# Optimization experiments

Hardware: AMD Instinct MI355X
Metric: run time of the kernel (lower is better)

Reference implementation:

```python
import jax, jax.numpy as jnp
import numpy as np

H, W, C = 256, 320, 28
HEADS, DH = 8, 28
K = 8   # DCT patch kernel (hardcoded in SpecDCT.forward)
WS = 8  # local attention window size
EPS = 1e-12


def _dct_mat(N):
    # torch_dct DCT-II with norm=None: X_k = 2 * sum_n x_n cos(pi*(2n+1)k/(2N))
    n = np.arange(N)
    D = 2.0 * np.cos(np.pi * (2.0 * n[None, :] + 1.0) * n[:, None] / (2.0 * N))
    return D.astype(np.float32)

_DHn = _dct_mat(H)
_DWn = _dct_mat(W)
D_H = jnp.asarray(_DHn)
D_W = jnp.asarray(_DWn)
DI_H = jnp.asarray(np.linalg.inv(_DHn).astype(np.float32))
DI_W = jnp.asarray(np.linalg.inv(_DWn).astype(np.float32))


def _l2norm(t):
    return t / jnp.maximum(jnp.linalg.norm(t, axis=-1, keepdims=True), EPS)


def _gelu(t):
    return jax.nn.gelu(t, approximate=False)


def _forward(x, spec_wq, spec_wk, spec_wv, spec_rescale, spec_proj_w, spec_proj_b,
             hf1_pw_w, hf1_dw_w, hf2_pw_w, coef_emb,
             loc_wq, loc_wkv, loc_pos, loc_proj_w, loc_proj_b, fus_w, fus_b):
    b = x.shape[0]
    hh, ww = H // K, W // K
    n = hh * ww
    mm = K * K
    # ---------- spectral DCT branch ----------
    x_nchw = x.transpose(0, 3, 1, 2)                                  # [b,C,H,W]
    x_dct = jnp.einsum('kh,bchw,lw->bckl', D_H, x_nchw, D_W)          # 2D DCT-II
    # patchify into 8x8 DCT blocks -> [b, n, mm, C]
    xt = x_dct.reshape(b, C, hh, K, ww, K).transpose(0, 2, 4, 3, 5, 1).reshape(b, n, mm, C)
    q = (xt @ spec_wq).reshape(b, n, mm, HEADS, DH).transpose(0, 1, 3, 4, 2)  # [b,n,h,d,mm]
    k = (xt @ spec_wk).reshape(b, n, mm, HEADS, DH).transpose(0, 1, 3, 4, 2)
    v = (xt @ spec_wv).reshape(b, n, mm, HEADS, DH).transpose(0, 1, 3, 4, 2)
    q = _l2norm(q)
    k = _l2norm(k)
    attn = jnp.einsum('bnhdm,bnhem->bnhde', q, k) * spec_rescale      # [b,n,h,d,d]
    attn = jax.nn.softmax(attn, axis=-1)
    x0 = jnp.einsum('bnhde,bnhem->bnhdm', attn, v)                    # [b,n,h,d,mm]
    x1 = x0.transpose(0, 1, 4, 2, 3).reshape(b, n, mm, HEADS * DH)
    x2 = x1 @ spec_proj_w + spec_proj_b                               # [b,n,mm,C]
    x_low = x2.reshape(b, hh, ww, K, K, C).transpose(0, 5, 1, 3, 2, 4).reshape(b, C, H, W)
    # high-frequency conv path (in DCT domain)
    y = _gelu(jnp.einsum('oc,bchw->bohw', hf1_pw_w, x_dct))
    y = _gelu(jax.lax.conv_general_dilated(
        y, hf1_dw_w, (1, 1), 'SAME', feature_group_count=C,
        dimension_numbers=('NCHW', 'OIHW', 'NCHW')))
    x_conv = y + x_dct
    x_high = _gelu(jnp.einsum('oc,bchw->bohw', hf2_pw_w, x_conv)) + x_conv
    coef = coef_emb[None, None]                                       # [1,1,H,W]
    x_out = coef * x_low + (1.0 - coef) * x_high + x_dct
    out_fd = jnp.einsum('kh,bchw,lw->bckl', DI_H, x_out, DI_W).transpose(0, 2, 3, 1)
    # ---------- windowed local attention branch ----------
    nh, nw = H // WS, W // WS
    xw = x.reshape(b, nh, WS, nw, WS, C).transpose(0, 1, 3, 2, 4, 5).reshape(b * nh * nw, WS * WS, C)
    ql = (xw @ loc_wq).reshape(-1, WS * WS, HEADS, DH).transpose(0, 2, 1, 3) * (DH ** -0.5)
    kv = xw @ loc_wkv
    kl = kv[..., :HEADS * DH].reshape(-1, WS * WS, HEADS, DH).transpose(0, 2, 1, 3)
    vl = kv[..., HEADS * DH:].reshape(-1, WS * WS, HEADS, DH).transpose(0, 2, 1, 3)
    sim = jnp.einsum('bhid,bhjd->bhij', ql, kl) + loc_pos
    a = jax.nn.softmax(sim, axis=-1)
    ol = jnp.einsum('bhij,bhjd->bhid', a, vl).transpose(0, 2, 1, 3).reshape(-1, WS * WS, HEADS * DH)
    ol = ol @ loc_proj_w + loc_proj_b
    out_local = ol.reshape(b, nh, nw, WS, WS, C).transpose(0, 1, 3, 2, 4, 5).reshape(b, H, W, C)
    # ---------- fusion (1x1 conv over concatenated channels) ----------
    sl = jnp.concatenate([out_fd, out_local], axis=-1)                # [b,H,W,2C]
    return jnp.einsum('oc,bhwc->bhwo', fus_w, sl) + fus_b


def setup_inputs():
    key = jax.random.key(0)
    ks = jax.random.split(key, 16)
    ID = HEADS * DH
    s = lambda i, shape, scale=0.02: jax.random.normal(ks[i], shape, jnp.float32) * scale
    return {
        'x': jax.random.normal(ks[0], (2, H, W, C), jnp.float32),
        'spec_wq': s(1, (C, ID)), 'spec_wk': s(2, (C, ID)), 'spec_wv': s(3, (C, ID)),
        'spec_rescale': jnp.ones((HEADS, 1, 1), jnp.float32),
        'spec_proj_w': s(4, (ID, C)), 'spec_proj_b': jnp.zeros((C,), jnp.float32),
        'hf1_pw_w': s(5, (C, C), 0.1), 'hf1_dw_w': s(6, (C, 1, 3, 3), 0.1),
        'hf2_pw_w': s(7, (C, C), 0.1),
        'coef_emb': jax.random.uniform(ks[8], (H, W), jnp.float32),
        'loc_wq': s(9, (C, ID)), 'loc_wkv': s(10, (C, 2 * ID)),
        'loc_pos': s(11, (1, HEADS, WS * WS, WS * WS), 1.0),
        'loc_proj_w': s(12, (ID, C)), 'loc_proj_b': jnp.zeros((C,), jnp.float32),
        'fus_w': s(13, (C, 2 * C)), 'fus_b': jnp.zeros((C,), jnp.float32),
    }


def reference(x, spec_wq, spec_wk, spec_wv, spec_rescale, spec_proj_w, spec_proj_b,
              hf1_pw_w, hf1_dw_w, hf2_pw_w, coef_emb,
              loc_wq, loc_wkv, loc_pos, loc_proj_w, loc_proj_b, fus_w, fus_b):
    return _forward(x, spec_wq, spec_wk, spec_wv, spec_rescale, spec_proj_w, spec_proj_b,
                    hf1_pw_w, hf1_dw_w, hf2_pw_w, coef_emb,
                    loc_wq, loc_wkv, loc_pos, loc_proj_w, loc_proj_b, fus_w, fus_b)
```

## Files before the change

### kernel.cpp

```cpp
#include <hip/hip_runtime.h>
#include <math.h>

#define H_ 256
#define W_ 320
#define C_ 28
#define HWC (H_ * W_ * C_)
#define PI_D 3.14159265358979323846

__device__ __forceinline__ float gelu_f(float x) {
    return 0.5f * x * (1.0f + erff(x * 0.7071067811865476f));
}

__global__ void gen_mats(float* __restrict__ dhT, float* __restrict__ dwT,
                         float* __restrict__ dihT, float* __restrict__ diwT) {
    int i = blockIdx.x * 256 + threadIdx.x;
    if (i < 256 * 256) {
        int k = i >> 8, n = i & 255;
        double c = cos(PI_D * (2.0 * n + 1.0) * k / 512.0);
        dhT[n * 256 + k] = (float)(2.0 * c);
        dihT[k * 256 + n] = (float)(k == 0 ? (1.0 / 512.0) : c / 256.0);
    }
    if (i < 320 * 320) {
        int k = i / 320, n = i - k * 320;
        double c = cos(PI_D * (2.0 * n + 1.0) * k / 640.0);
        dwT[n * 320 + k] = (float)(2.0 * c);
        diwT[k * 320 + n] = (float)(k == 0 ? (1.0 / 640.0) : c / 320.0);
    }
}

__global__ void gen_locG(const float* __restrict__ wq, const float* __restrict__ wkv,
                         float* __restrict__ G) {
    int i = blockIdx.x * 256 + threadIdx.x;
    if (i < 6272) {
        int h = i / 784, r = i - h * 784;
        int c = r / 28, cp = r - c * 28;
        float s = 0.f;
        #pragma unroll
        for (int d = 0; d < 28; ++d)
            s += wq[c * 224 + h * 28 + d] * wkv[cp * 448 + h * 28 + d];
        G[i] = s * 0.18898223650461363f;
    }
}

__global__ void gen_locM2(const float* __restrict__ wkv, const float* __restrict__ pw,
                          float* __restrict__ M2) {
    int i = blockIdx.x * 256 + threadIdx.x;
    if (i < 6272) {
        int h = i / 784, r = i - h * 784;
        int c = r / 28, co = r - c * 28;
        float s = 0.f;
        #pragma unroll
        for (int d = 0; d < 28; ++d)
            s += wkv[c * 448 + 224 + h * 28 + d] * pw[(h * 28 + d) * 28 + co];
        M2[i] = s;
    }
}

__global__ void gen_posT(const float* __restrict__ pos, float* __restrict__ posT) {
    int id = blockIdx.x * 256 + threadIdx.x;
    int h = id >> 12, r = id & 4095, i = r >> 6, j = r & 63;
    posT[(h << 12) + (j << 6) + i] = pos[id];
}

__global__ void dct_apply(const float* __restrict__ matT, const float* __restrict__ in,
                          float* __restrict__ out, int M, int Kd, int inner_n,
                          int stride_i_in, int kstride_in,
                          int stride_i_out, int mstride_out) {
    extern __shared__ float s_in[];
    int bidx = blockIdx.x;
    int o = bidx / inner_n;
    int ii = bidx - o * inner_n;
    const float* bin = in + (size_t)o * HWC + (size_t)ii * stride_i_in;
    float* bout = out + (size_t)o * HWC + (size_t)ii * stride_i_out;
    int tot = Kd * C_;
    for (int e = threadIdx.x; e < tot; e += blockDim.x) {
        int k = e / C_;
        int c = e - k * C_;
        s_in[e] = bin[k * kstride_in + c];
    }
    __syncthreads();
    int m = threadIdx.x;
    if (m < M) {
        float4 acc[7];
        #pragma unroll
        for (int q = 0; q < 7; ++q) acc[q] = make_float4(0.f, 0.f, 0.f, 0.f);
        for (int k = 0; k < Kd; ++k) {
            float d = matT[k * M + m];
            const float4* row = (const float4*)(s_in + k * C_);
            #pragma unroll
            for (int q = 0; q < 7; ++q) {
                float4 v = row[q];
                acc[q].x += d * v.x; acc[q].y += d * v.y;
                acc[q].z += d * v.z; acc[q].w += d * v.w;
            }
        }
        float4* orow = (float4*)(bout + (size_t)m * mstride_out);
        #pragma unroll
        for (int q = 0; q < 7; ++q) orow[q] = acc[q];
    }
}

__global__ __launch_bounds__(256, 4) void spec_attn(
    const float* __restrict__ xdct, const float* __restrict__ wq,
    const float* __restrict__ wk, const float* __restrict__ wv,
    const float* __restrict__ rescale, const float* __restrict__ pw,
    const float* __restrict__ pb, float* __restrict__ xlow) {
    __shared__ __align__(16) float smem[9780];
    float* sX  = smem;
    float* sG  = sX + 1856;
    float* sWq = sG + 784;
    float* sWk = sWq + 784;
    float* sWv = sWk + 784;
    float* sPw = sWv + 784;
    float* sA  = sPw + 784;
    float* sB  = sA + 784;
    float* sP  = sB + 784;
    float* sM3 = sP + 812;
    float* sR  = sM3 + 784;
    float* sqn = sR + 784;
    float* skn = sqn + 28;

    int t = threadIdx.x;
    int blk = blockIdx.x;
    int b = blk / 1280;
    int r = blk - b * 1280;
    int bh = r / 40;
    int bw = r - bh * 40;
    const float* base = xdct + ((size_t)((b * 256 + bh * 8) * 320 + bw * 8)) * 28;

    for (int e = t; e < 1792; e += 256) {
        int m = e / 28, c = e - m * 28;
        sX[m * 29 + c] = base[((m >> 3) * 320 + (m & 7)) * 28 + c];
    }
    for (int e = t; e < 784; e += 256) sR[e] = 0.f;
    __syncthreads();

    for (int e = t; e < 784; e += 256) {
        int c = e / 28, c2 = e - c * 28;
        float a0 = 0.f, a1 = 0.f, a2 = 0.f, a3 = 0.f;
        #pragma unroll 4
        for (int m = 0; m < 64; m += 4) {
            a0 += sX[m * 29 + c] * sX[m * 29 + c2];
            a1 += sX[(m + 1) * 29 + c] * sX[(m + 1) * 29 + c2];
            a2 += sX[(m + 2) * 29 + c] * sX[(m + 2) * 29 + c2];
            a3 += sX[(m + 3) * 29 + c] * sX[(m + 3) * 29 + c2];
        }
        sG[e] = (a0 + a1) + (a2 + a3);
    }
    __syncthreads();

    for (int h = 0; h < 8; ++h) {
        for (int e = t; e < 784; e += 256) {
            int c = e / 28, d = e - c * 28;
            sWq[e] = wq[c * 224 + h * 28 + d];
            sWk[e] = wk[c * 224 + h * 28 + d];
            sWv[e] = wv[c * 224 + h * 28 + d];
            sPw[e] = pw[h * 784 + e];
        }
        __syncthreads();
        for (int tile = t; tile < 392; tile += 256) {
            int isB = tile >= 196;
            int tt = isB ? tile - 196 : tile;
            int c = tt / 7, d4 = (tt - c * 7) * 4;
            const float* W = isB ? sWk : sWq;
            float ax = 0.f, ay = 0.f, az = 0.f, aw = 0.f;
            #pragma unroll
            for (int c2 = 0; c2 < 28; ++c2) {
                float g = sG[c * 28 + c2];
                const float4 w4 = *(const float4*)(W + c2 * 28 + d4);
                ax += g * w4.x; ay += g * w4.y; az += g * w4.z; aw += g * w4.w;
            }
            float* dst = (isB ? sB : sA) + c * 28 + d4;
            *(float4*)dst = make_float4(ax, ay, az, aw);
        }
        __syncthreads();
        if (t < 28) {
            float s = 0.f;
            #pragma unroll
            for (int c = 0; c < 28; ++c) s += sWq[c * 28 + t] * sA[c * 28 + t];
            sqn[t] = fmaxf(sqrtf(s), 1e-12f);
        } else if (t >= 32 && t < 60) {
            int d = t - 32;
            float s = 0.f;
            #pragma unroll
            for (int c = 0; c < 28; ++c) s += sWk[c * 28 + d] * sB[c * 28 + d];
            skn[d] = fmaxf(sqrtf(s), 1e-12f);
        }
        __syncthreads();
        float resc = rescale[h];
        for (int e = t; e < 784; e += 256) {
            int d = e / 28, ee = e - d * 28;
            float s = 0.f;
            #pragma unroll
            for (int c = 0; c < 28; ++c) s += sWq[c * 28 + d] * sB[c * 28 + ee];
            sP[d * 29 + ee] = __expf(s * resc / (sqn[d] * skn[ee]));
        }
        __syncthreads();
        if (t < 28) {
            float s = 0.f;
            #pragma unroll
            for (int ee = 0; ee < 28; ++ee) s += sP[t * 29 + ee];
            float inv = 1.0f / s;
            #pragma unroll
            for (int ee = 0; ee < 28; ++ee) sP[t * 29 + ee] *= inv;
        }
        __syncthreads();
        for (int id = t; id < 784; id += 256) {
            int ee = id / 28, co = id - ee * 28;
            float a0 = 0.f, a1 = 0.f;
            #pragma unroll 2
            for (int d = 0; d < 28; d += 2) {
                a0 += sP[d * 29 + ee] * sPw[d * 28 + co];
                a1 += sP[(d + 1) * 29 + ee] * sPw[(d + 1) * 28 + co];
            }
            sM3[id] = a0 + a1;
        }
        __syncthreads();
        for (int id = t; id < 784; id += 256) {
            int c = id / 28, co = id - c * 28;
            float a0 = 0.f, a1 = 0.f;
            #pragma unroll 2
            for (int e = 0; e < 28; e += 2) {
                a0 += sWv[c * 28 + e] * sM3[e * 28 + co];
                a1 += sWv[c * 28 + e + 1] * sM3[(e + 1) * 28 + co];
            }
            sR[id] += a0 + a1;
        }
        __syncthreads();
    }
    float* outp = xlow + ((size_t)((b * 256 + bh * 8) * 320 + bw * 8)) * 28;
    for (int id = t; id < 1792; id += 256) {
        int m = id / 28, co = id - m * 28;
        float s = pb[co];
        #pragma unroll
        for (int c = 0; c < 28; ++c) s += sX[m * 29 + c] * sR[c * 28 + co];
        outp[((m >> 3) * 320 + (m & 7)) * 28 + co] = s;
    }
}

__global__ __launch_bounds__(256) void hf_pw1(const float* __restrict__ xdct,
                                              const float* __restrict__ w,
                                              float* __restrict__ y1) {
    __shared__ float s_w[28][29];
    __shared__ float s_x[256][29];
    int t = threadIdx.x;
    for (int e = t; e < 784; e += 256) s_w[e / 28][e % 28] = w[e];
    size_t p0 = (size_t)blockIdx.x * 256;
    const float* src = xdct + p0 * 28;
    for (int e = t; e < 7168; e += 256) {
        int p = e / 28, c = e - p * 28;
        s_x[p][c] = src[e];
    }
    __syncthreads();
    float o[28];
    #pragma unroll
    for (int oo = 0; oo < 28; ++oo) {
        float a = 0.f;
        #pragma unroll
        for (int c = 0; c < 28; ++c) a += s_w[oo][c] * s_x[t][c];
        o[oo] = gelu_f(a);
    }
    __syncthreads();
    #pragma unroll
    for (int oo = 0; oo < 28; ++oo) s_x[t][oo] = o[oo];
    __syncthreads();
    float* dst = y1 + p0 * 28;
    for (int e = t; e < 7168; e += 256) {
        int p = e / 28, c = e - p * 28;
        dst[e] = s_x[p][c];
    }
}

__global__ __launch_bounds__(256) void hf_combine(
    const float* __restrict__ y1, const float* __restrict__ xdct,
    const float* __restrict__ xlow, const float* __restrict__ dww,
    const float* __restrict__ pw2, const float* __restrict__ coef,
    float* __restrict__ xout) {
    __shared__ float s_dw[252];
    __shared__ float s_pw[28][29];
    int t = threadIdx.x;
    for (int e = t; e < 252; e += 256) s_dw[e] = dww[e];
    for (int e = t; e < 784; e += 256) s_pw[e / 28][e % 28] = pw2[e];
    __syncthreads();
    int pix = blockIdx.x * 256 + t;
    int b = pix / 81920;
    int rem = pix - b * 81920;
    int y = rem / 320;
    int xx = rem - y * 320;
    float conv[28];
    #pragma unroll
    for (int c = 0; c < 28; ++c) conv[c] = 0.f;
    for (int dy = 0; dy < 3; ++dy) {
        int yy = y + dy - 1;
        if (yy < 0 || yy >= 256) continue;
        for (int dx = 0; dx < 3; ++dx) {
            int xq = xx + dx - 1;
            if (xq < 0 || xq >= 320) continue;
            const float* rp = y1 + ((size_t)(b * 256 + yy) * 320 + xq) * 28;
            #pragma unroll
            for (int c = 0; c < 28; ++c) conv[c] += s_dw[c * 9 + dy * 3 + dx] * rp[c];
        }
    }
    const float* xd = xdct + (size_t)pix * 28;
    const float* xl = xlow + (size_t)pix * 28;
    float xdr[28], xcv[28];
    #pragma unroll
    for (int c = 0; c < 28; ++c) {
        xdr[c] = xd[c];
        xcv[c] = gelu_f(conv[c]) + xdr[c];
    }
    float cf = coef[rem];
    float omc = 1.0f - cf;
    float* xo = xout + (size_t)pix * 28;
    #pragma unroll
    for (int oo = 0; oo < 28; ++oo) {
        float a = 0.f;
        #pragma unroll
        for (int c = 0; c < 28; ++c) a += s_pw[oo][c] * xcv[c];
        float xh = gelu_f(a) + xcv[oo];
        xo[oo] = cf * xl[oo] + omc * xh + xdr[oo];
    }
}

__global__ __launch_bounds__(256, 2) void local_attn(
    const float* __restrict__ x, const float* __restrict__ G,
    const float* __restrict__ M2, const float* __restrict__ posT,
    const float* __restrict__ pb, float* __restrict__ outloc) {
    __shared__ float s_G[8 * 784];
    __shared__ float s_M2[8 * 784];
    __shared__ float s_xw[4 * 64 * 28];
    int t = threadIdx.x;
    int wave = t >> 6, lane = t & 63;
    for (int e = t; e < 6272; e += 256) { s_G[e] = G[e]; s_M2[e] = M2[e]; }
    int win = blockIdx.x * 4 + wave;
    int b = win / 1280;
    int r = win - b * 1280;
    int wh = r / 40, wwi = r - wh * 40;
    int p_ = lane >> 3, q_ = lane & 7;
    const float* rowp = x + ((size_t)((b * 256 + wh * 8 + p_) * 320) + wwi * 8 + q_) * 28;
    float xw[28];
    float* sxw_mine = s_xw + (wave * 64 + lane) * 28;
    #pragma unroll
    for (int q4 = 0; q4 < 7; ++q4) {
        float4 v4 = ((const float4*)rowp)[q4];
        xw[4 * q4] = v4.x; xw[4 * q4 + 1] = v4.y; xw[4 * q4 + 2] = v4.z; xw[4 * q4 + 3] = v4.w;
        ((float4*)sxw_mine)[q4] = v4;
    }
    __syncthreads();
    float acc[28];
    #pragma unroll
    for (int c = 0; c < 28; ++c) acc[c] = 0.f;
    const float* swbase = s_xw + wave * 1792;
    for (int h = 0; h < 8; ++h) {
        float t1[28];
        #pragma unroll
        for (int d = 0; d < 28; ++d) t1[d] = 0.f;
        const float* gh = s_G + h * 784;
        #pragma unroll
        for (int c = 0; c < 28; ++c) {
            float xc = xw[c];
            const float* gr = gh + c * 28;
            #pragma unroll
            for (int d = 0; d < 28; ++d) t1[d] += xc * gr[d];
        }
        float S = 0.f;
        float u[28];
        #pragma unroll
        for (int c = 0; c < 28; ++c) u[c] = 0.f;
        const float* pbase = posT + (h << 12) + lane;
        for (int j = 0; j < 64; ++j) {
            const float4* rj = (const float4*)(swbase + j * 28);
            float rr[28];
            #pragma unroll
            for (int q4 = 0; q4 < 7; ++q4) {
                float4 v4 = rj[q4];
                rr[4 * q4] = v4.x; rr[4 * q4 + 1] = v4.y;
                rr[4 * q4 + 2] = v4.z; rr[4 * q4 + 3] = v4.w;
            }
            float a0 = 0.f, a1 = 0.f, a2 = 0.f, a3 = 0.f;
            #pragma unroll
            for (int c = 0; c < 28; c += 4) {
                a0 += t1[c] * rr[c];
                a1 += t1[c + 1] * rr[c + 1];
                a2 += t1[c + 2] * rr[c + 2];
                a3 += t1[c + 3] * rr[c + 3];
            }
            float s = ((a0 + a1) + (a2 + a3)) + pbase[j << 6];
            float p = __expf(s);
            S += p;
            #pragma unroll
            for (int c = 0; c < 28; ++c) u[c] += p * rr[c];
        }
        float inv = 1.0f / S;
        const float* mh = s_M2 + h * 784;
        #pragma unroll
        for (int c = 0; c < 28; ++c) {
            float uc = u[c] * inv;
            const float* mr = mh + c * 28;
            #pragma unroll
            for (int co = 0; co < 28; ++co) acc[co] += uc * mr[co];
        }
    }
    float* op = outloc + ((size_t)((b * 256 + wh * 8 + p_) * 320) + wwi * 8 + q_) * 28;
    #pragma unroll
    for (int q4 = 0; q4 < 7; ++q4) {
        float4 o4;
        o4.x = acc[4 * q4] + pb[4 * q4];
        o4.y = acc[4 * q4 + 1] + pb[4 * q4 + 1];
        o4.z = acc[4 * q4 + 2] + pb[4 * q4 + 2];
        o4.w = acc[4 * q4 + 3] + pb[4 * q4 + 3];
        ((float4*)op)[q4] = o4;
    }
}

__global__ __launch_bounds__(256) void fuse_k(
    const float* __restrict__ fd, const float* __restrict__ loc,
    const float* __restrict__ w, const float* __restrict__ bias,
    float* __restrict__ out) {
    __shared__ float s_w[28][57];
    __shared__ float s_b[28];
    int t = threadIdx.x;
    for (int e = t; e < 28 * 56; e += 256) s_w[e / 56][e % 56] = w[e];
    if (t < 28) s_b[t] = bias[t];
    __syncthreads();
    size_t pix = (size_t)blockIdx.x * 256 + t;
    const float* f = fd + pix * 28;
    const float* l = loc + pix * 28;
    float fr[28], lr[28];
    #pragma unroll
    for (int c = 0; c < 28; ++c) { fr[c] = f[c]; lr[c] = l[c]; }
    float* o = out + pix * 28;
    #pragma unroll
    for (int oo = 0; oo < 28; ++oo) {
        float a = s_b[oo];
        #pragma unroll
        for (int c = 0; c < 28; ++c) a += s_w[oo][c] * fr[c] + s_w[oo][28 + c] * lr[c];
        o[oo] = a;
    }
}

extern "C" void kernel_launch(void* const* d_in, const int* in_sizes, int n_in,
                              void* d_out, int out_size, void* d_ws, size_t ws_size,
                              hipStream_t stream) {
    const float* x         = (const float*)d_in[0];
    const float* spec_wq   = (const float*)d_in[1];
    const float* spec_wk   = (const float*)d_in[2];
    const float* spec_wv   = (const float*)d_in[3];
    const float* spec_resc = (const float*)d_in[4];
    const float* spec_pw   = (const float*)d_in[5];
    const float* spec_pb   = (const float*)d_in[6];
    const float* hf1_pw_w  = (const float*)d_in[7];
    const float* hf1_dw_w  = (const float*)d_in[8];
    const float* hf2_pw_w  = (const float*)d_in[9];
    const float* coef_emb  = (const float*)d_in[10];
    const float* loc_wq    = (const float*)d_in[11];
    const float* loc_wkv   = (const float*)d_in[12];
    const float* loc_pos   = (const float*)d_in[13];
    const float* loc_pw    = (const float*)d_in[14];
    const float* loc_pb    = (const float*)d_in[15];
    const float* fus_w     = (const float*)d_in[16];
    const float* fus_b     = (const float*)d_in[17];

    float* ws = (float*)d_ws;
    float* mDH  = ws;
    float* mDW  = mDH + 65536;
    float* mDIH = mDW + 102400;
    float* mDIW = mDIH + 65536;
    float* locG = mDIW + 102400;
    float* locM2 = locG + 6272;
    float* posT = locM2 + 6272;
    float* bufA = posT + 32768;
    float* bufB = bufA + 2 * HWC;
    float* bufC = bufB + 2 * HWC;
    float* bufD = bufC + 2 * HWC;

    gen_mats<<<400, 256, 0, stream>>>(mDH, mDW, mDIH, mDIW);
    gen_locG<<<25, 256, 0, stream>>>(loc_wq, loc_wkv, locG);
    gen_locM2<<<25, 256, 0, stream>>>(loc_wkv, loc_pw, locM2);
    gen_posT<<<128, 256, 0, stream>>>(loc_pos, posT);

    dct_apply<<<640, 256, 256 * 28 * 4, stream>>>(mDH, x, bufA,
        256, 256, 320, 28, 8960, 28, 8960);
    dct_apply<<<512, 320, 320 * 28 * 4, stream>>>(mDW, bufA, bufB,
        320, 320, 256, 8960, 28, 8960, 28);

    spec_attn<<<2560, 256, 0, stream>>>(bufB, spec_wq, spec_wk, spec_wv,
                                        spec_resc, spec_pw, spec_pb, bufC);
    hf_pw1<<<640, 256, 0, stream>>>(bufB, hf1_pw_w, bufA);
    hf_combine<<<640, 256, 0, stream>>>(bufA, bufB, bufC, hf1_dw_w, hf2_pw_w,
                                        coef_emb, bufD);
    dct_apply<<<640, 256, 256 * 28 * 4, stream>>>(mDIH, bufD, bufA,
        256, 256, 320, 28, 8960, 28, 8960);
    dct_apply<<<512, 320, 320 * 28 * 4, stream>>>(mDIW, bufA, bufC,
        320, 320, 256, 8960, 28, 8960, 28);

    local_attn<<<640, 256, 0, stream>>>(x, locG, locM2, posT, loc_pb, bufB);

    fuse_k<<<640, 256, 0, stream>>>(bufC, bufB, fus_w, fus_b, (float*)d_out);
}
```

Before: 1.185 ms.

## Split local attention heads across two waves per window and drop shared weight staging

The local attention kernel now assigns two waves to each window, each handling four of the eight heads. Their partial outputs are combined through shared memory before the store, and the grid doubles to match. The G and M2 weight matrices are no longer copied into shared memory. They are read straight from global memory with float4 loads, which cuts LDS use and allows a higher occupancy hint. The cost is an extra block barrier, a shared-memory reduction, and weight reads that now depend on the cache.

Result: slower. 1.251 ms (+5.6%).

```diff
diff --git a/kernel.cpp b/kernel.cpp
--- a/kernel.cpp
+++ b/kernel.cpp
@@ -322,52 +322,56 @@
     }
 }
 
-__global__ __launch_bounds__(256, 2) void local_attn(
+__global__ __launch_bounds__(256, 3) void local_attn(
     const float* __restrict__ x, const float* __restrict__ G,
     const float* __restrict__ M2, const float* __restrict__ posT,
     const float* __restrict__ pb, float* __restrict__ outloc) {
-    __shared__ float s_G[8 * 784];
-    __shared__ float s_M2[8 * 784];
-    __shared__ float s_xw[4 * 64 * 28];
+    __shared__ float s_xw[2][1792];
+    __shared__ float s_part[2][1792];
     int t = threadIdx.x;
     int wave = t >> 6, lane = t & 63;
-    for (int e = t; e < 6272; e += 256) { s_G[e] = G[e]; s_M2[e] = M2[e]; }
-    int win = blockIdx.x * 4 + wave;
+    int wi = wave >> 1, hg = wave & 1;
+    int win = blockIdx.x * 2 + wi;
     int b = win / 1280;
     int r = win - b * 1280;
     int wh = r / 40, wwi = r - wh * 40;
     int p_ = lane >> 3, q_ = lane & 7;
     const float* rowp = x + ((size_t)((b * 256 + wh * 8 + p_) * 320) + wwi * 8 + q_) * 28;
     float xw[28];
-    float* sxw_mine = s_xw + (wave * 64 + lane) * 28;
     #pragma unroll
     for (int q4 = 0; q4 < 7; ++q4) {
         float4 v4 = ((const float4*)rowp)[q4];
         xw[4 * q4] = v4.x; xw[4 * q4 + 1] = v4.y; xw[4 * q4 + 2] = v4.z; xw[4 * q4 + 3] = v4.w;
-        ((float4*)sxw_mine)[q4] = v4;
+        if (hg == 0) ((float4*)(s_xw[wi] + lane * 28))[q4] = v4;
     }
     __syncthreads();
     float acc[28];
     #pragma unroll
     for (int c = 0; c < 28; ++c) acc[c] = 0.f;
-    const float* swbase = s_xw + wave * 1792;
-    for (int h = 0; h < 8; ++h) {
+    const float* swbase = s_xw[wi];
+    for (int hh = 0; hh < 4; ++hh) {
+        int h = hg * 4 + hh;
         float t1[28];
         #pragma unroll
         for (int d = 0; d < 28; ++d) t1[d] = 0.f;
-        const float* gh = s_G + h * 784;
+        const float* gh = G + h * 784;
         #pragma unroll
         for (int c = 0; c < 28; ++c) {
             float xc = xw[c];
-            const float* gr = gh + c * 28;
-            #pragma unroll
-            for (int d = 0; d < 28; ++d) t1[d] += xc * gr[d];
+            const float4* gr = (const float4*)(gh + c * 28);
+            #pragma unroll
+            for (int q4 = 0; q4 < 7; ++q4) {
+                float4 g4 = gr[q4];
+                t1[4 * q4] += xc * g4.x; t1[4 * q4 + 1] += xc * g4.y;
+                t1[4 * q4 + 2] += xc * g4.z; t1[4 * q4 + 3] += xc * g4.w;
+            }
         }
         float S = 0.f;
         float u[28];
         #pragma unroll
         for (int c = 0; c < 28; ++c) u[c] = 0.f;
         const float* pbase = posT + (h << 12) + lane;
+        #pragma unroll 2
         for (int j = 0; j < 64; ++j) {
             const float4* rj = (const float4*)(swbase + j * 28);
             float rr[28];
@@ -392,24 +396,39 @@
             for (int c = 0; c < 28; ++c) u[c] += p * rr[c];
         }
         float inv = 1.0f / S;
-        const float* mh = s_M2 + h * 784;
+        const float* mh = M2 + h * 784;
         #pragma unroll
         for (int c = 0; c < 28; ++c) {
             float uc = u[c] * inv;
-            const float* mr = mh + c * 28;
-            #pragma unroll
-            for (int co = 0; co < 28; ++co) acc[co] += uc * mr[co];
-        }
-    }
-    float* op = outloc + ((size_t)((b * 256 + wh * 8 + p_) * 320) + wwi * 8 + q_) * 28;
-    #pragma unroll
-    for (int q4 = 0; q4 < 7; ++q4) {
-        float4 o4;
-        o4.x = acc[4 * q4] + pb[4 * q4];
-        o4.y = acc[4 * q4 + 1] + pb[4 * q4 + 1];
-        o4.z = acc[4 * q4 + 2] + pb[4 * q4 + 2];
-        o4.w = acc[4 * q4 + 3] + pb[4 * q4 + 3];
-        ((float4*)op)[q4] = o4;
+            const float4* mr = (const float4*)(mh + c * 28);
+            #pragma unroll
+            for (int q4 = 0; q4 < 7; ++q4) {
+                float4 m4 = mr[q4];
+                acc[4 * q4] += uc * m4.x; acc[4 * q4 + 1] += uc * m4.y;
+                acc[4 * q4 + 2] += uc * m4.z; acc[4 * q4 + 3] += uc * m4.w;
+            }
+        }
+    }
+    if (hg == 1) {
+        float4* dst = (float4*)(s_part[wi] + lane * 28);
+        #pragma unroll
+        for (int q4 = 0; q4 < 7; ++q4)
+            dst[q4] = make_float4(acc[4 * q4], acc[4 * q4 + 1], acc[4 * q4 + 2], acc[4 * q4 + 3]);
+    }
+    __syncthreads();
+    if (hg == 0) {
+        const float4* pr = (const float4*)(s_part[wi] + lane * 28);
+        float* op = outloc + ((size_t)((b * 256 + wh * 8 + p_) * 320) + wwi * 8 + q_) * 28;
+        #pragma unroll
+        for (int q4 = 0; q4 < 7; ++q4) {
+            float4 p4 = pr[q4];
+            float4 o4;
+            o4.x = acc[4 * q4] + p4.x + pb[4 * q4];
+            o4.y = acc[4 * q4 + 1] + p4.y + pb[4 * q4 + 1];
+            o4.z = acc[4 * q4 + 2] + p4.z + pb[4 * q4 + 2];
+            o4.w = acc[4 * q4 + 3] + p4.w + pb[4 * q4 + 3];
+            ((float4*)op)[q4] = o4;
+        }
     }
 }
 
@@ -494,7 +513,7 @@
     dct_apply<<<512, 320, 320 * 28 * 4, stream>>>(mDIW, bufA, bufC,
         320, 320, 256, 8960, 28, 8960, 28);
 
-    local_attn<<<640, 256, 0, stream>>>(x, locG, locM2, posT, loc_pb, bufB);
+    local_attn<<<1280, 256, 0, stream>>>(x, locG, locM2, posT, loc_pb, bufB);
 
     fuse_k<<<640, 256, 0, stream>>>(bufC, bufB, fus_w, fus_b, (float*)d_out);
 }
```

## Restructure local attention to one window per block with shared staged matmuls

Applied to the files above, without the earlier changes.

Rewrites the local window attention kernel so each 256-thread block handles one 8x8 window instead of one window per wave. It stages the projection T, the probability matrix P and its row sums in shared memory, and splits work across threads as small cooperative matmuls separated by barriers. G and M2 are now read from global memory rather than copied into shared memory, and the pos transpose kernel is dropped in favour of reading pos directly. This aims to cut the large per-thread register arrays and raise occupancy, at the cost of many more __syncthreads per head and more global and uncached reads of the weight matrices.

Result: slower. 1.543 ms (+30.2%).

```diff
diff --git a/kernel.cpp b/kernel.cpp
--- a/kernel.cpp
+++ b/kernel.cpp
@@ -54,12 +54,6 @@
             s += wkv[c * 448 + 224 + h * 28 + d] * pw[(h * 28 + d) * 28 + co];
         M2[i] = s;
     }
-}
-
-__global__ void gen_posT(const float* __restrict__ pos, float* __restrict__ posT) {
-    int id = blockIdx.x * 256 + threadIdx.x;
-    int h = id >> 12, r = id & 4095, i = r >> 6, j = r & 63;
-    posT[(h << 12) + (j << 6) + i] = pos[id];
 }
 
 __global__ void dct_apply(const float* __restrict__ matT, const float* __restrict__ in,
@@ -322,94 +316,104 @@
     }
 }
 
-__global__ __launch_bounds__(256, 2) void local_attn(
+__global__ __launch_bounds__(256) void local_attn(
     const float* __restrict__ x, const float* __restrict__ G,
-    const float* __restrict__ M2, const float* __restrict__ posT,
+    const float* __restrict__ M2, const float* __restrict__ pos,
     const float* __restrict__ pb, float* __restrict__ outloc) {
-    __shared__ float s_G[8 * 784];
-    __shared__ float s_M2[8 * 784];
-    __shared__ float s_xw[4 * 64 * 28];
+    __shared__ float sXw[64 * 29];
+    __shared__ float sT[64 * 29];
+    __shared__ float sP[64 * 65];
+    __shared__ float sSum[64 * 4];
     int t = threadIdx.x;
-    int wave = t >> 6, lane = t & 63;
-    for (int e = t; e < 6272; e += 256) { s_G[e] = G[e]; s_M2[e] = M2[e]; }
-    int win = blockIdx.x * 4 + wave;
+    int win = blockIdx.x;
     int b = win / 1280;
     int r = win - b * 1280;
     int wh = r / 40, wwi = r - wh * 40;
-    int p_ = lane >> 3, q_ = lane & 7;
-    const float* rowp = x + ((size_t)((b * 256 + wh * 8 + p_) * 320) + wwi * 8 + q_) * 28;
-    float xw[28];
-    float* sxw_mine = s_xw + (wave * 64 + lane) * 28;
-    #pragma unroll
-    for (int q4 = 0; q4 < 7; ++q4) {
-        float4 v4 = ((const float4*)rowp)[q4];
-        xw[4 * q4] = v4.x; xw[4 * q4 + 1] = v4.y; xw[4 * q4 + 2] = v4.z; xw[4 * q4 + 3] = v4.w;
-        ((float4*)sxw_mine)[q4] = v4;
-    }
-    __syncthreads();
-    float acc[28];
-    #pragma unroll
-    for (int c = 0; c < 28; ++c) acc[c] = 0.f;
-    const float* swbase = s_xw + wave * 1792;
+    const float* base = x + ((size_t)((b * 256 + wh * 8) * 320) + wwi * 8) * 28;
+    for (int e = t; e < 1792; e += 256) {
+        int i = e / 28, c = e - i * 28;
+        sXw[i * 29 + c] = base[((i >> 3) * 320 + (i & 7)) * 28 + c];
+    }
+    float acc[7];
+    #pragma unroll
+    for (int q = 0; q < 7; ++q) acc[q] = 0.f;
+    __syncthreads();
+
+    int row = t >> 2;
+    int j0 = (t & 3) << 4;
     for (int h = 0; h < 8; ++h) {
-        float t1[28];
-        #pragma unroll
-        for (int d = 0; d < 28; ++d) t1[d] = 0.f;
-        const float* gh = s_G + h * 784;
-        #pragma unroll
-        for (int c = 0; c < 28; ++c) {
-            float xc = xw[c];
-            const float* gr = gh + c * 28;
-            #pragma unroll
-            for (int d = 0; d < 28; ++d) t1[d] += xc * gr[d];
-        }
-        float S = 0.f;
-        float u[28];
-        #pragma unroll
-        for (int c = 0; c < 28; ++c) u[c] = 0.f;
-        const float* pbase = posT + (h << 12) + lane;
-        for (int j = 0; j < 64; ++j) {
-            const float4* rj = (const float4*)(swbase + j * 28);
-            float rr[28];
-            #pragma unroll
-            for (int q4 = 0; q4 < 7; ++q4) {
-                float4 v4 = rj[q4];
-                rr[4 * q4] = v4.x; rr[4 * q4 + 1] = v4.y;
-                rr[4 * q4 + 2] = v4.z; rr[4 * q4 + 3] = v4.w;
-            }
+        const float* gh = G + h * 784;
+        #pragma unroll
+        for (int q = 0; q < 7; ++q) {
+            int e = q * 256 + t;
+            int i = e / 28, d = e - i * 28;
+            float a0 = 0.f, a1 = 0.f;
+            #pragma unroll 2
+            for (int c = 0; c < 28; c += 2) {
+                a0 += sXw[i * 29 + c] * gh[c * 28 + d];
+                a1 += sXw[i * 29 + c + 1] * gh[(c + 1) * 28 + d];
+            }
+            sT[i * 29 + d] = a0 + a1;
+        }
+        __syncthreads();
+        {
+            const float* ph = pos + ((h << 6) + row) * 64;
+            float psum = 0.f;
+            #pragma unroll 4
+            for (int jj = 0; jj < 16; ++jj) {
+                int j = j0 + jj;
+                float a0 = 0.f, a1 = 0.f, a2 = 0.f, a3 = 0.f;
+                #pragma unroll
+                for (int c = 0; c < 28; c += 4) {
+                    a0 += sT[row * 29 + c] * sXw[j * 29 + c];
+                    a1 += sT[row * 29 + c + 1] * sXw[j * 29 + c + 1];
+                    a2 += sT[row * 29 + c + 2] * sXw[j * 29 + c + 2];
+                    a3 += sT[row * 29 + c + 3] * sXw[j * 29 + c + 3];
+                }
+                float p = __expf(((a0 + a1) + (a2 + a3)) + ph[j]);
+                sP[row * 65 + j] = p;
+                psum += p;
+            }
+            sSum[(row << 2) + (t & 3)] = psum;
+        }
+        __syncthreads();
+        #pragma unroll
+        for (int q = 0; q < 7; ++q) {
+            int e = q * 256 + t;
+            int i = e / 28, c = e - i * 28;
+            float inv = 1.0f / (sSum[i * 4] + sSum[i * 4 + 1] + sSum[i * 4 + 2] + sSum[i * 4 + 3]);
             float a0 = 0.f, a1 = 0.f, a2 = 0.f, a3 = 0.f;
-            #pragma unroll
-            for (int c = 0; c < 28; c += 4) {
-                a0 += t1[c] * rr[c];
-                a1 += t1[c + 1] * rr[c + 1];
-                a2 += t1[c + 2] * rr[c + 2];
-                a3 += t1[c + 3] * rr[c + 3];
-            }
-            float s = ((a0 + a1) + (a2 + a3)) + pbase[j << 6];
-            float p = __expf(s);
-            S += p;
-            #pragma unroll
-            for (int c = 0; c < 28; ++c) u[c] += p * rr[c];
-        }
-        float inv = 1.0f / S;
-        const float* mh = s_M2 + h * 784;
-        #pragma unroll
-        for (int c = 0; c < 28; ++c) {
-            float uc = u[c] * inv;
-            const float* mr = mh + c * 28;
-            #pragma unroll
-            for (int co = 0; co < 28; ++co) acc[co] += uc * mr[co];
-        }
-    }
-    float* op = outloc + ((size_t)((b * 256 + wh * 8 + p_) * 320) + wwi * 8 + q_) * 28;
-    #pragma unroll
-    for (int q4 = 0; q4 < 7; ++q4) {
-        float4 o4;
-        o4.x = acc[4 * q4] + pb[4 * q4];
-        o4.y = acc[4 * q4 + 1] + pb[4 * q4 + 1];
-        o4.z = acc[4 * q4 + 2] + pb[4 * q4 + 2];
-        o4.w = acc[4 * q4 + 3] + pb[4 * q4 + 3];
-        ((float4*)op)[q4] = o4;
+            #pragma unroll 4
+            for (int j = 0; j < 64; j += 4) {
+                a0 += sP[i * 65 + j] * sXw[j * 29 + c];
+                a1 += sP[i * 65 + j + 1] * sXw[(j + 1) * 29 + c];
+                a2 += sP[i * 65 + j + 2] * sXw[(j + 2) * 29 + c];
+                a3 += sP[i * 65 + j + 3] * sXw[(j + 3) * 29 + c];
+            }
+            sT[i * 29 + c] = ((a0 + a1) + (a2 + a3)) * inv;
+        }
+        __syncthreads();
+        const float* mh = M2 + h * 784;
+        #pragma unroll
+        for (int q = 0; q < 7; ++q) {
+            int e = q * 256 + t;
+            int i = e / 28, c = e - i * 28;
+            float a0 = 0.f, a1 = 0.f;
+            #pragma unroll 2
+            for (int d = 0; d < 28; d += 2) {
+                a0 += sT[i * 29 + d] * mh[d * 28 + c];
+                a1 += sT[i * 29 + d + 1] * mh[(d + 1) * 28 + c];
+            }
+            acc[q] += a0 + a1;
+        }
+        __syncthreads();
+    }
+    float* op = outloc + ((size_t)((b * 256 + wh * 8) * 320) + wwi * 8) * 28;
+    #pragma unroll
+    for (int q = 0; q < 7; ++q) {
+        int e = q * 256 + t;
+        int i = e / 28, c = e - i * 28;
+        op[((i >> 3) * 320 + (i & 7)) * 28 + c] = acc[q] + pb[c];
     }
 }
 
@@ -468,8 +472,7 @@
     float* mDIW = mDIH + 65536;
     float* locG = mDIW + 102400;
     float* locM2 = locG + 6272;
-    float* posT = locM2 + 6272;
-    float* bufA = posT + 32768;
+    float* bufA = locM2 + 6272;
     float* bufB = bufA + 2 * HWC;
     float* bufC = bufB + 2 * HWC;
     float* bufD = bufC + 2 * HWC;
@@ -477,7 +480,6 @@
     gen_mats<<<400, 256, 0, stream>>>(mDH, mDW, mDIH, mDIW);
     gen_locG<<<25, 256, 0, stream>>>(loc_wq, loc_wkv, locG);
     gen_locM2<<<25, 256, 0, stream>>>(loc_wkv, loc_pw, locM2);
-    gen_posT<<<128, 256, 0, stream>>>(loc_pos, posT);
 
     dct_apply<<<640, 256, 256 * 28 * 4, stream>>>(mDH, x, bufA,
         256, 256, 320, 28, 8960, 28, 8960);
@@ -494,7 +496,7 @@
     dct_apply<<<512, 320, 320 * 28 * 4, stream>>>(mDIW, bufA, bufC,
         320, 320, 256, 8960, 28, 8960, 28);
 
-    local_attn<<<640, 256, 0, stream>>>(x, locG, locM2, posT, loc_pb, bufB);
+    local_attn<<<2560, 256, 0, stream>>>(x, locG, locM2, loc_pos, loc_pb, bufB);
 
     fuse_k<<<640, 256, 0, stream>>>(bufC, bufB, fus_w, fus_b, (float*)d_out);
 }
```
